# Performance work log

Measured on AMD Instinct MI355X. Metric: run time of the kernel, lower is better.

Reference implementation:

```python
import jax, jax.numpy as jnp
import numpy as np

NUM_HEADS = 28
HEAD_DIM = 128
NUM_KV_HEADS = 4
N_REP = NUM_HEADS // NUM_KV_HEADS  # 7
ROPE_THETA = 1000000.0
CUR_IND = 0  # prefill into empty cache
_K_MASK = float(jnp.finfo(jnp.bfloat16).min)


def _rope_sincos(position_ids, head_dim, theta):
    # position_ids: (B, T) int -> sin, cos: (B, T, head_dim//2)
    half = head_dim // 2
    fraction = jnp.arange(half, dtype=jnp.float32) / half
    timescale = theta ** fraction  # (half,)
    ang = position_ids[..., None].astype(jnp.float32) / timescale
    return jnp.sin(ang), jnp.cos(ang)


def _apply_rope(x, sin, cos):
    # x: (B, T, N, H); sin/cos: (B, T, H//2)
    half = x.shape[-1] // 2
    x1, x2 = x[..., :half], x[..., half:]
    s, c = sin[:, :, None, :], cos[:, :, None, :]
    return jnp.concatenate([x1 * c - x2 * s, x2 * c + x1 * s], axis=-1).astype(x.dtype)


def setup_inputs() -> dict:
    key = jax.random.key(0)
    ks = jax.random.split(key, 8)
    B, T, D = 2, 1024, 3584
    KVD = NUM_KV_HEADS * HEAD_DIM  # 512
    sd = 1.0 / np.sqrt(D)
    return {
        "x": jax.random.normal(ks[0], (B, T, D), jnp.float32),
        "segment_ids": jnp.ones((B, T), jnp.int32),
        "k_cache": jnp.zeros((B, T, NUM_KV_HEADS, HEAD_DIM), jnp.float32),
        "v_cache": jnp.zeros((B, T, NUM_KV_HEADS, HEAD_DIM), jnp.float32),
        "Wq": jax.random.normal(ks[1], (D, D), jnp.float32) * sd,
        "bq": jax.random.normal(ks[2], (D,), jnp.float32) * 0.01,
        "Wk": jax.random.normal(ks[3], (D, KVD), jnp.float32) * sd,
        "bk": jax.random.normal(ks[4], (KVD,), jnp.float32) * 0.01,
        "Wv": jax.random.normal(ks[5], (D, KVD), jnp.float32) * sd,
        "bv": jax.random.normal(ks[6], (KVD,), jnp.float32) * 0.01,
        "Wo": jax.random.normal(ks[7], (D, D), jnp.float32) * sd,
    }


def reference(x, segment_ids, k_cache, v_cache, Wq, bq, Wk, bk, Wv, bv, Wo):
    b, t, _ = x.shape
    cache_size = k_cache.shape[1]
    scale = HEAD_DIM ** -0.5

    q = (x @ Wq + bq).reshape(b, t, NUM_HEADS, HEAD_DIM)
    k = (x @ Wk + bk).reshape(b, t, NUM_KV_HEADS, HEAD_DIM)
    v = (x @ Wv + bv).reshape(b, t, NUM_KV_HEADS, HEAD_DIM)

    # left pads and positions (cache.start_ind initialized <0 -> becomes left_pads)
    valid = segment_ids != 0
    left_pads = jnp.sum(jnp.cumsum(valid, axis=-1) == 0, axis=-1).astype(jnp.int32)  # (B,)
    start_ind = left_pads
    position_ids = (jnp.cumsum(valid, axis=-1) - 1).astype(jnp.int32) + CUR_IND  # (B, T)

    sin, cos = _rope_sincos(position_ids, HEAD_DIM, ROPE_THETA)
    q = _apply_rope(q, sin, cos)
    k = _apply_rope(k, sin, cos)

    # write into KV cache at cur_ind (prefill: overwrites [0:t])
    k_cache = jax.lax.dynamic_update_slice(k_cache, k, (0, CUR_IND, 0, 0))
    v_cache = jax.lax.dynamic_update_slice(v_cache, v, (0, CUR_IND, 0, 0))

    q_gqa = q.reshape(b, t, NUM_KV_HEADS, N_REP, HEAD_DIM)
    attn_logits = jnp.einsum('BTKGH,BSKH->BTSKG', q_gqa, k_cache) * scale

    q_pos = CUR_IND + jnp.arange(t, dtype=jnp.int32)[None, :] - start_ind[:, None]  # (B,T)
    ts = jnp.arange(cache_size, dtype=jnp.int32)
    kv_segment_ids = (ts[None, :] >= start_ind[:, None]) & (ts[None, :] < CUR_IND + t)  # (B,S)
    k_pos = ts[None, :] - start_ind[:, None]  # (B,S)
    causal_mask = k_pos[:, None, :] <= q_pos[:, :, None]          # (B,T,S)
    segment_mask = kv_segment_ids[:, None, :] == segment_ids[:, :, None]  # (B,T,S)
    final_mask = (causal_mask & segment_mask)[:, :, :, None, None]  # (B,T,S,1,1)

    attn_logits = jnp.where(final_mask, attn_logits, _K_MASK)
    attn_weights = jax.nn.softmax(attn_logits.astype(jnp.float32), axis=2).astype(attn_logits.dtype)

    qkv = jnp.einsum('BTSKG,BSKH->BTKGH', attn_weights, v_cache)
    qkv = qkv.reshape(b, t, NUM_HEADS * HEAD_DIM)
    return qkv @ Wo
```

## Files before the change

kernel.cpp:

```cpp
#include <hip/hip_runtime.h>
#include <hip/hip_bf16.h>
#include <stdint.h>

#define T_SEQ 1024
#define DMODEL 3584
#define KVDIM 512
#define NQH 28
#define NKVH 4
#define NREP 7
#define HD 128
#define NTOT 4608
#define BATCH 2
#define MROWS 2048
#define KMASK (-3.3895314e38f)

typedef __attribute__((ext_vector_type(8))) short short8;
typedef __attribute__((ext_vector_type(4))) float f32x4;

#define SB()       asm volatile("s_barrier" ::: "memory")
#define WAIT_VM0() asm volatile("s_waitcnt vmcnt(0)" ::: "memory")

__device__ __forceinline__ short8 ld_s8(const __hip_bfloat16* p) {
    return *reinterpret_cast<const short8*>(p);
}

__device__ __forceinline__ f32x4 mfma16(short8 a, short8 b, f32x4 c) {
    return __builtin_amdgcn_mfma_f32_16x16x32_bf16(a, b, c, 0, 0, 0);
}

__device__ __forceinline__ void gload_lds16(const __hip_bfloat16* g, __hip_bfloat16* l) {
    __builtin_amdgcn_global_load_lds(
        (const __attribute__((address_space(1))) unsigned int*)g,
        (__attribute__((address_space(3))) unsigned int*)l,
        16, 0, 0);
}

__global__ void scan_kernel(const int* __restrict__ seg, int* __restrict__ pos_ids,
                            int* __restrict__ left_pads) {
    int b = blockIdx.x;
    int t = threadIdx.x;
    __shared__ int cum[T_SEQ];
    __shared__ int lp;
    if (t == 0) lp = 0;
    cum[t] = (seg[b * T_SEQ + t] != 0) ? 1 : 0;
    __syncthreads();
    for (int off = 1; off < T_SEQ; off <<= 1) {
        int add = (t >= off) ? cum[t - off] : 0;
        __syncthreads();
        cum[t] += add;
        __syncthreads();
    }
    pos_ids[b * T_SEQ + t] = cum[t] - 1;
    if (cum[t] == 0) atomicAdd(&lp, 1);
    __syncthreads();
    if (t == 0) left_pads[b] = lp;
}

__global__ void convert_bf16(const float* __restrict__ x, __hip_bfloat16* __restrict__ xb, int n) {
    int i = (blockIdx.x * blockDim.x + threadIdx.x) * 4;
    if (i >= n) return;
    float4 v = *reinterpret_cast<const float4*>(x + i);
    union { __hip_bfloat16 h[4]; uint2 u; } o;
    o.h[0] = __float2bfloat16(v.x);
    o.h[1] = __float2bfloat16(v.y);
    o.h[2] = __float2bfloat16(v.z);
    o.h[3] = __float2bfloat16(v.w);
    *reinterpret_cast<uint2*>(xb + i) = o.u;
}

__global__ void transpose_convert(const float* __restrict__ W, __hip_bfloat16* __restrict__ WT,
                                  int K, int N) {
    __shared__ float tile[32][33];
    int n0 = blockIdx.x * 32, k0 = blockIdx.y * 32;
    int tx = threadIdx.x, ty = threadIdx.y;
#pragma unroll
    for (int j = 0; j < 4; j++)
        tile[ty + j * 8][tx] = W[(size_t)(k0 + ty + j * 8) * N + n0 + tx];
    __syncthreads();
#pragma unroll
    for (int j = 0; j < 4; j++)
        WT[(size_t)(n0 + ty + j * 8) * K + k0 + tx] = __float2bfloat16(tile[tx][ty + j * 8]);
}

__global__ void transpose_v(const __hip_bfloat16* __restrict__ qkv, __hip_bfloat16* __restrict__ vbT) {
    __shared__ __hip_bfloat16 tile[32][33];
    int c0 = blockIdx.x * 32;
    int s0 = blockIdx.y * 32;
    int b = blockIdx.z;
    int tx = threadIdx.x, ty = threadIdx.y;
#pragma unroll
    for (int j = 0; j < 4; j++)
        tile[ty + j * 8][tx] = qkv[(size_t)(b * T_SEQ + s0 + ty + j * 8) * NTOT + DMODEL + KVDIM + c0 + tx];
    __syncthreads();
#pragma unroll
    for (int j = 0; j < 4; j++)
        vbT[((size_t)b * KVDIM + c0 + ty + j * 8) * T_SEQ + s0 + tx] = tile[tx][ty + j * 8];
}

__global__ void rope_kernel(__hip_bfloat16* __restrict__ qkv, const int* __restrict__ pos_ids) {
    int row = blockIdx.x;
    int tid = threadIdx.x;
    __shared__ float sc[2][64];
    float fpos = (float)pos_ids[row];
    if (tid < 64) {
        float freq = exp2f((float)tid * (-0.31143076632024816f));
        float ang = fpos * freq;
        sc[0][tid] = sinf(ang);
        sc[1][tid] = cosf(ang);
    }
    __syncthreads();
    __hip_bfloat16* rp = qkv + (size_t)row * NTOT;
    for (int p = tid; p < 32 * 64; p += 256) {
        int hh = p >> 6;
        int j = p & 63;
        int cb = (hh < NQH) ? hh * HD : DMODEL + (hh - NQH) * HD;
        float s = sc[0][j], c = sc[1][j];
        float x1 = __bfloat162float(rp[cb + j]);
        float x2 = __bfloat162float(rp[cb + j + 64]);
        rp[cb + j] = __float2bfloat16(x1 * c - x2 * s);
        rp[cb + j + 64] = __float2bfloat16(x2 * c + x1 * s);
    }
}

template <int MODE>
__global__ __launch_bounds__(512, 2) void gemm256(
    const __hip_bfloat16* __restrict__ A, const __hip_bfloat16* __restrict__ BT,
    int M, int N, int K, int nbx,
    const float* __restrict__ bq, const float* __restrict__ bk, const float* __restrict__ bv,
    __hip_bfloat16* __restrict__ Cb, float* __restrict__ Cf) {
    __shared__ __hip_bfloat16 As[2][256 * 64];
    __shared__ __hip_bfloat16 Bs[2][256 * 64];
    int tid = threadIdx.x;
    int wv = tid >> 6, lane = tid & 63;
    int wr = wv >> 2, wc = wv & 3;
    int r16 = lane & 15, g4 = lane >> 4;
    int nwg = gridDim.x;
    int sb = ((int)blockIdx.x & 7) * (nwg >> 3) + ((int)blockIdx.x >> 3);
    int bx = sb % nbx, by = sb / nbx;
    int bm = by * 256, bn = bx * 256;
    int nt = K >> 6;

    int lrow = lane >> 3;
    int srcoff = ((lane & 7) * 8) ^ (lrow * 8);

    auto stageA = [&](int buf, int t) {
        const __hip_bfloat16* src = A + (size_t)t * 64 + srcoff;
#pragma unroll
        for (int h = 0; h < 2; h++)
#pragma unroll
            for (int i = 0; i < 2; i++) {
                int r0 = h * 128 + wv * 16 + i * 8;
                gload_lds16(src + (size_t)(bm + r0 + lrow) * K, &As[buf][r0 * 64]);
            }
    };
    auto stageB = [&](int buf, int t) {
        const __hip_bfloat16* src = BT + (size_t)t * 64 + srcoff;
#pragma unroll
        for (int h = 0; h < 2; h++)
#pragma unroll
            for (int i = 0; i < 2; i++) {
                int r0 = h * 128 + wv * 16 + i * 8;
                gload_lds16(src + (size_t)(bn + r0 + lrow) * K, &Bs[buf][r0 * 64]);
            }
    };
    int swz = (r16 & 7) << 3;

    f32x4 acc[8][4] = {};
    stageA(0, 0);
    stageB(0, 0);

    for (int w = 0; w < nt; w++) {
        int buf = w & 1;
        WAIT_VM0();
        SB();
        short8 aF[4][2], bF0[2][2], bF1[2][2];
#pragma unroll
        for (int mi = 0; mi < 4; mi++)
#pragma unroll
            for (int ks = 0; ks < 2; ks++) {
                int row = wr * 128 + mi * 16 + r16;
                aF[mi][ks] = ld_s8(&As[buf][row * 64 + ((ks * 32 + g4 * 8) ^ swz)]);
            }
#pragma unroll
        for (int ni = 0; ni < 2; ni++)
#pragma unroll
            for (int ks = 0; ks < 2; ks++) {
                int row = wc * 64 + ni * 16 + r16;
                bF0[ni][ks] = ld_s8(&Bs[buf][row * 64 + ((ks * 32 + g4 * 8) ^ swz)]);
            }
        if (w + 1 < nt) stageA(buf ^ 1, w + 1);
        SB();
        __builtin_amdgcn_s_setprio(1);
#pragma unroll
        for (int mi = 0; mi < 4; mi++)
#pragma unroll
            for (int ni = 0; ni < 2; ni++) {
                acc[mi][ni] = mfma16(aF[mi][0], bF0[ni][0], acc[mi][ni]);
                acc[mi][ni] = mfma16(aF[mi][1], bF0[ni][1], acc[mi][ni]);
            }
        __builtin_amdgcn_s_setprio(0);
        SB();
#pragma unroll
        for (int ni = 0; ni < 2; ni++)
#pragma unroll
            for (int ks = 0; ks < 2; ks++) {
                int row = wc * 64 + (2 + ni) * 16 + r16;
                bF1[ni][ks] = ld_s8(&Bs[buf][row * 64 + ((ks * 32 + g4 * 8) ^ swz)]);
            }
        if (w + 1 < nt) stageB(buf ^ 1, w + 1);
        SB();
        __builtin_amdgcn_s_setprio(1);
#pragma unroll
        for (int mi = 0; mi < 4; mi++)
#pragma unroll
            for (int ni = 0; ni < 2; ni++) {
                acc[mi][2 + ni] = mfma16(aF[mi][0], bF1[ni][0], acc[mi][2 + ni]);
                acc[mi][2 + ni] = mfma16(aF[mi][1], bF1[ni][1], acc[mi][2 + ni]);
            }
        __builtin_amdgcn_s_setprio(0);
        SB();
#pragma unroll
        for (int mi = 0; mi < 4; mi++)
#pragma unroll
            for (int ks = 0; ks < 2; ks++) {
                int row = wr * 128 + 64 + mi * 16 + r16;
                aF[mi][ks] = ld_s8(&As[buf][row * 64 + ((ks * 32 + g4 * 8) ^ swz)]);
            }
        SB();
        __builtin_amdgcn_s_setprio(1);
#pragma unroll
        for (int mi = 0; mi < 4; mi++)
#pragma unroll
            for (int ni = 0; ni < 2; ni++) {
                acc[4 + mi][ni] = mfma16(aF[mi][0], bF0[ni][0], acc[4 + mi][ni]);
                acc[4 + mi][ni] = mfma16(aF[mi][1], bF0[ni][1], acc[4 + mi][ni]);
            }
        __builtin_amdgcn_s_setprio(0);
        SB();
        __builtin_amdgcn_s_setprio(1);
#pragma unroll
        for (int mi = 0; mi < 4; mi++)
#pragma unroll
            for (int ni = 0; ni < 2; ni++) {
                acc[4 + mi][2 + ni] = mfma16(aF[mi][0], bF1[ni][0], acc[4 + mi][2 + ni]);
                acc[4 + mi][2 + ni] = mfma16(aF[mi][1], bF1[ni][1], acc[4 + mi][2 + ni]);
            }
        __builtin_amdgcn_s_setprio(0);
    }
#pragma unroll
    for (int m = 0; m < 8; m++) {
#pragma unroll
        for (int n = 0; n < 4; n++) {
            int row0 = bm + wr * 128 + m * 16 + g4 * 4;
            int col = bn + wc * 64 + n * 16 + r16;
            float badd = 0.0f;
            if (MODE == 0)
                badd = (col < DMODEL) ? bq[col]
                       : (col < DMODEL + KVDIM ? bk[col - DMODEL] : bv[col - DMODEL - KVDIM]);
#pragma unroll
            for (int reg = 0; reg < 4; reg++) {
                float v = acc[m][n][reg] + badd;
                if (MODE == 0)
                    Cb[(size_t)(row0 + reg) * N + col] = __float2bfloat16(v);
                else
                    Cf[(size_t)(row0 + reg) * N + col] = v;
            }
        }
    }
}

__global__ __launch_bounds__(448, 4) void attn_kernel(
    const __hip_bfloat16* __restrict__ qkv, const __hip_bfloat16* __restrict__ vbT,
    const int* __restrict__ seg, const int* __restrict__ left_pads,
    __hip_bfloat16* __restrict__ attn_out) {
    int qt_raw = blockIdx.x;
    int kvh = blockIdx.y;
    int b = blockIdx.z;
    int qt = (b == 1) ? 63 - qt_raw : qt_raw;
    int tid = threadIdx.x;
    int w = tid >> 6;
    int lane = tid & 63;
    int r = lane & 15, g = lane >> 4;
    int h = kvh * NREP + w;
    int start = left_pads[b];
    const float scale = 0.08838834764831845f;

    __shared__ __hip_bfloat16 Kt[2][64 * 128];
    __shared__ __hip_bfloat16 Vt[2][128 * 64];
    __shared__ __hip_bfloat16 Ps[NREP][16 * 64];

    const __hip_bfloat16* Qp = qkv + (size_t)(b * T_SEQ + qt * 16 + r) * NTOT + h * HD;
    short8 qf[4];
#pragma unroll
    for (int kc = 0; kc < 4; kc++) qf[kc] = ld_s8(Qp + kc * 32 + g * 8);

    int qrow = qt * 16 + r;
    int segq = seg[b * T_SEQ + qrow];
    int qpos = qrow - start;

    float m_run = -__builtin_inff();
    float l_part = 0.0f;
    f32x4 acc[8] = {};

    const __hip_bfloat16* Kg = qkv + (size_t)(b * T_SEQ) * NTOT + DMODEL + kvh * HD;
    const __hip_bfloat16* Vg = vbT + ((size_t)b * KVDIM + kvh * HD) * T_SEQ;
    int nt = qt / 4 + 1;

    auto stage = [&](int buf, int t) {
        int s0 = t * 64;
        for (int i = w; i < 16; i += NREP) {
            int slot = i * 64 + lane;
            int row = slot >> 4;
            int c = ((slot & 15) << 4) ^ ((row & 7) << 4);
            gload_lds16(Kg + (size_t)(s0 + row) * NTOT + (c >> 1), &Kt[buf][i * 512]);
        }
        for (int i = w; i < 16; i += NREP) {
            int slot = i * 64 + lane;
            int d = slot >> 3;
            int c = ((slot & 7) << 4) ^ ((d & 7) << 4);
            gload_lds16(Vg + (size_t)d * T_SEQ + s0 + (c >> 1), &Vt[buf][i * 512]);
        }
    };

    stage(0, 0);
    __syncthreads();
    int buf = 0;
    for (int t = 0; t < nt; t++) {
        if (t + 1 < nt) stage(buf ^ 1, t + 1);
        int s0 = t * 64;
        f32x4 sacc[4] = {};
#pragma unroll
        for (int n = 0; n < 4; n++) {
#pragma unroll
            for (int kc = 0; kc < 4; kc++) {
                int col = (kc * 32 + g * 8) ^ ((r & 7) << 3);
                short8 kf = ld_s8(&Kt[buf][(n * 16 + r) * 128 + col]);
                sacc[n] = mfma16(kf, qf[kc], sacc[n]);
            }
        }
        float p[16];
        float mt = -__builtin_inff();
#pragma unroll
        for (int n = 0; n < 4; n++)
#pragma unroll
            for (int reg = 0; reg < 4; reg++) {
                int kv = s0 + n * 16 + g * 4 + reg;
                float val = sacc[n][reg] * scale;
                bool ok = (kv - start <= qpos) && (((kv >= start) ? 1 : 0) == segq);
                val = ok ? val : KMASK;
                p[n * 4 + reg] = val;
                mt = fmaxf(mt, val);
            }
        mt = fmaxf(mt, __shfl_xor(mt, 16, 64));
        mt = fmaxf(mt, __shfl_xor(mt, 32, 64));
        if (!__all(mt <= m_run + 8.0f)) {
            float mn = fmaxf(m_run, mt);
            float fac = __expf(m_run - mn);
            m_run = mn;
            l_part *= fac;
            float facr[4];
#pragma unroll
            for (int reg = 0; reg < 4; reg++) facr[reg] = __shfl(fac, g * 4 + reg, 64);
#pragma unroll
            for (int h7 = 0; h7 < 8; h7++)
#pragma unroll
                for (int reg = 0; reg < 4; reg++)
                    acc[h7][reg] *= facr[reg];
        }
#pragma unroll
        for (int i = 0; i < 16; i++) {
            p[i] = __expf(p[i] - m_run);
            l_part += p[i];
        }
#pragma unroll
        for (int n = 0; n < 4; n++) {
            union { __hip_bfloat16 h[4]; uint2 u; } pk;
#pragma unroll
            for (int reg = 0; reg < 4; reg++) pk.h[reg] = __float2bfloat16(p[n * 4 + reg]);
            int col = (n * 16 + g * 4) ^ ((r & 7) << 3);
            *reinterpret_cast<uint2*>(&Ps[w][r * 64 + col]) = pk.u;
        }
#pragma unroll
        for (int kc = 0; kc < 2; kc++) {
            int colp = (kc * 32 + g * 8) ^ ((r & 7) << 3);
            short8 a_pv = ld_s8(&Ps[w][r * 64 + colp]);
#pragma unroll
            for (int h7 = 0; h7 < 8; h7++) {
                int d = h7 * 16 + r;
                int colv = (kc * 32 + g * 8) ^ ((r & 7) << 3);
                short8 vf = ld_s8(&Vt[buf][d * 64 + colv]);
                acc[h7] = mfma16(a_pv, vf, acc[h7]);
            }
        }
        __syncthreads();
        buf ^= 1;
    }
    l_part += __shfl_xor(l_part, 16, 64);
    l_part += __shfl_xor(l_part, 32, 64);
    float invl[4];
#pragma unroll
    for (int reg = 0; reg < 4; reg++) invl[reg] = 1.0f / __shfl(l_part, g * 4 + reg, 64);
#pragma unroll
    for (int h7 = 0; h7 < 8; h7++)
#pragma unroll
        for (int reg = 0; reg < 4; reg++)
            attn_out[(size_t)(b * T_SEQ + qt * 16 + g * 4 + reg) * DMODEL + h * HD + h7 * 16 + r] =
                __float2bfloat16(acc[h7][reg] * invl[reg]);
}

extern "C" void kernel_launch(void* const* d_in, const int* in_sizes, int n_in,
                              void* d_out, int out_size, void* d_ws, size_t ws_size,
                              hipStream_t stream) {
    const float* x = (const float*)d_in[0];
    const int* seg = (const int*)d_in[1];
    const float* Wq = (const float*)d_in[4];
    const float* bq = (const float*)d_in[5];
    const float* Wk = (const float*)d_in[6];
    const float* bk = (const float*)d_in[7];
    const float* Wv = (const float*)d_in[8];
    const float* bv = (const float*)d_in[9];
    const float* Wo = (const float*)d_in[10];
    float* out = (float*)d_out;

    uint8_t* ws = (uint8_t*)d_ws;
    size_t off = 0;
    auto alloc = [&](size_t bytes) -> void* {
        void* p = ws + off;
        off += (bytes + 255) & ~(size_t)255;
        return p;
    };
    int* pos_ids = (int*)alloc(MROWS * sizeof(int));
    int* left_pads = (int*)alloc(16 * sizeof(int));
    __hip_bfloat16* xb = (__hip_bfloat16*)alloc((size_t)MROWS * DMODEL * 2);
    __hip_bfloat16* WqkvT = (__hip_bfloat16*)alloc((size_t)NTOT * DMODEL * 2);
    __hip_bfloat16* WoT = (__hip_bfloat16*)alloc((size_t)DMODEL * DMODEL * 2);
    __hip_bfloat16* qkv = (__hip_bfloat16*)alloc((size_t)MROWS * NTOT * 2);
    __hip_bfloat16* vbT = (__hip_bfloat16*)alloc((size_t)BATCH * KVDIM * T_SEQ * 2);
    __hip_bfloat16* attn = (__hip_bfloat16*)alloc((size_t)MROWS * DMODEL * 2);

    scan_kernel<<<BATCH, T_SEQ, 0, stream>>>(seg, pos_ids, left_pads);
    convert_bf16<<<(MROWS * DMODEL / 4 + 255) / 256, 256, 0, stream>>>(x, xb, MROWS * DMODEL);
    transpose_convert<<<dim3(DMODEL / 32, DMODEL / 32), dim3(32, 8), 0, stream>>>(Wq, WqkvT, DMODEL, DMODEL);
    transpose_convert<<<dim3(KVDIM / 32, DMODEL / 32), dim3(32, 8), 0, stream>>>(
        Wk, WqkvT + (size_t)DMODEL * DMODEL, DMODEL, KVDIM);
    transpose_convert<<<dim3(KVDIM / 32, DMODEL / 32), dim3(32, 8), 0, stream>>>(
        Wv, WqkvT + (size_t)(DMODEL + KVDIM) * DMODEL, DMODEL, KVDIM);
    transpose_convert<<<dim3(DMODEL / 32, DMODEL / 32), dim3(32, 8), 0, stream>>>(Wo, WoT, DMODEL, DMODEL);
    gemm256<0><<<dim3((NTOT / 256) * (MROWS / 256)), 512, 0, stream>>>(
        xb, WqkvT, MROWS, NTOT, DMODEL, NTOT / 256, bq, bk, bv, qkv, nullptr);
    rope_kernel<<<MROWS, 256, 0, stream>>>(qkv, pos_ids);
    transpose_v<<<dim3(KVDIM / 32, T_SEQ / 32, BATCH), dim3(32, 8), 0, stream>>>(qkv, vbT);
    attn_kernel<<<dim3(T_SEQ / 16, NKVH, BATCH), 448, 0, stream>>>(qkv, vbT, seg, left_pads, attn);
    gemm256<1><<<dim3((DMODEL / 256) * (MROWS / 256)), 512, 0, stream>>>(
        attn, WoT, MROWS, DMODEL, DMODEL, DMODEL / 256, nullptr, nullptr, nullptr, nullptr, out);
}
```

Baseline: 469.7 us.

## Retile GEMMs to 128xBN tiles sized so grids exactly fill 256 CUs

Replaces the fixed 256x256, 8-wave GEMM with a templated 128xBN kernel: BN=288 with 9 waves for the QKV projection and BN=224 with 7 waves for the output projection. Each launch is exactly 256 workgroups, matching the MI355X CU count, which removes the partial-wave tail of the old 144- and 112-block grids. Each wave now covers a 128x32 output slice instead of 128x64, so there are fewer MFMAs per LDS fragment load and less data reuse. Launch bounds drop to one block per SM.

```diff
diff --git a/kernel.cpp b/kernel.cpp
--- a/kernel.cpp
+++ b/kernel.cpp
@@ -122,22 +122,24 @@
     }
 }
 
-template <int MODE>
-__global__ __launch_bounds__(512, 2) void gemm256(
+template <int BN, int NW, int MODE>
+__global__ __launch_bounds__(NW * 64, 1) void gemmX(
     const __hip_bfloat16* __restrict__ A, const __hip_bfloat16* __restrict__ BT,
     int M, int N, int K, int nbx,
     const float* __restrict__ bq, const float* __restrict__ bk, const float* __restrict__ bv,
     __hip_bfloat16* __restrict__ Cb, float* __restrict__ Cf) {
-    __shared__ __hip_bfloat16 As[2][256 * 64];
-    __shared__ __hip_bfloat16 Bs[2][256 * 64];
+    constexpr int BM = 128;
+    constexpr int NCHA = BM / 8;
+    constexpr int NCHB = BN / 8;
+    __shared__ __hip_bfloat16 As[2][BM * 64];
+    __shared__ __hip_bfloat16 Bs[2][BN * 64];
     int tid = threadIdx.x;
     int wv = tid >> 6, lane = tid & 63;
-    int wr = wv >> 2, wc = wv & 3;
     int r16 = lane & 15, g4 = lane >> 4;
     int nwg = gridDim.x;
     int sb = ((int)blockIdx.x & 7) * (nwg >> 3) + ((int)blockIdx.x >> 3);
     int bx = sb % nbx, by = sb / nbx;
-    int bm = by * 256, bn = bx * 256;
+    int bm = by * BM, bn = bx * BN;
     int nt = K >> 6;
 
     int lrow = lane >> 3;
@@ -146,26 +148,24 @@
     auto stageA = [&](int buf, int t) {
         const __hip_bfloat16* src = A + (size_t)t * 64 + srcoff;
 #pragma unroll
-        for (int h = 0; h < 2; h++)
-#pragma unroll
-            for (int i = 0; i < 2; i++) {
-                int r0 = h * 128 + wv * 16 + i * 8;
-                gload_lds16(src + (size_t)(bm + r0 + lrow) * K, &As[buf][r0 * 64]);
-            }
+        for (int c = 0; c < NCHA; c += NW) {
+            int cc = c + wv;
+            if (cc < NCHA)
+                gload_lds16(src + (size_t)(bm + cc * 8 + lrow) * K, &As[buf][cc * 512]);
+        }
     };
     auto stageB = [&](int buf, int t) {
         const __hip_bfloat16* src = BT + (size_t)t * 64 + srcoff;
 #pragma unroll
-        for (int h = 0; h < 2; h++)
-#pragma unroll
-            for (int i = 0; i < 2; i++) {
-                int r0 = h * 128 + wv * 16 + i * 8;
-                gload_lds16(src + (size_t)(bn + r0 + lrow) * K, &Bs[buf][r0 * 64]);
-            }
+        for (int c = 0; c < NCHB; c += NW) {
+            int cc = c + wv;
+            if (cc < NCHB)
+                gload_lds16(src + (size_t)(bn + cc * 8 + lrow) * K, &Bs[buf][cc * 512]);
+        }
     };
     int swz = (r16 & 7) << 3;
 
-    f32x4 acc[8][4] = {};
+    f32x4 acc[8][2] = {};
     stageA(0, 0);
     stageB(0, 0);
 
@@ -173,21 +173,17 @@
         int buf = w & 1;
         WAIT_VM0();
         SB();
-        short8 aF[4][2], bF0[2][2], bF1[2][2];
+        short8 aLo[4][2], aHi[4][2], bF[2][2];
 #pragma unroll
         for (int mi = 0; mi < 4; mi++)
 #pragma unroll
-            for (int ks = 0; ks < 2; ks++) {
-                int row = wr * 128 + mi * 16 + r16;
-                aF[mi][ks] = ld_s8(&As[buf][row * 64 + ((ks * 32 + g4 * 8) ^ swz)]);
-            }
+            for (int ks = 0; ks < 2; ks++)
+                aLo[mi][ks] = ld_s8(&As[buf][(mi * 16 + r16) * 64 + ((ks * 32 + g4 * 8) ^ swz)]);
 #pragma unroll
         for (int ni = 0; ni < 2; ni++)
 #pragma unroll
-            for (int ks = 0; ks < 2; ks++) {
-                int row = wc * 64 + ni * 16 + r16;
-                bF0[ni][ks] = ld_s8(&Bs[buf][row * 64 + ((ks * 32 + g4 * 8) ^ swz)]);
-            }
+            for (int ks = 0; ks < 2; ks++)
+                bF[ni][ks] = ld_s8(&Bs[buf][(wv * 32 + ni * 16 + r16) * 64 + ((ks * 32 + g4 * 8) ^ swz)]);
         if (w + 1 < nt) stageA(buf ^ 1, w + 1);
         SB();
         __builtin_amdgcn_s_setprio(1);
@@ -195,18 +191,16 @@
         for (int mi = 0; mi < 4; mi++)
 #pragma unroll
             for (int ni = 0; ni < 2; ni++) {
-                acc[mi][ni] = mfma16(aF[mi][0], bF0[ni][0], acc[mi][ni]);
-                acc[mi][ni] = mfma16(aF[mi][1], bF0[ni][1], acc[mi][ni]);
+                acc[mi][ni] = mfma16(aLo[mi][0], bF[ni][0], acc[mi][ni]);
+                acc[mi][ni] = mfma16(aLo[mi][1], bF[ni][1], acc[mi][ni]);
             }
         __builtin_amdgcn_s_setprio(0);
         SB();
 #pragma unroll
-        for (int ni = 0; ni < 2; ni++)
-#pragma unroll
-            for (int ks = 0; ks < 2; ks++) {
-                int row = wc * 64 + (2 + ni) * 16 + r16;
-                bF1[ni][ks] = ld_s8(&Bs[buf][row * 64 + ((ks * 32 + g4 * 8) ^ swz)]);
-            }
+        for (int mi = 0; mi < 4; mi++)
+#pragma unroll
+            for (int ks = 0; ks < 2; ks++)
+                aHi[mi][ks] = ld_s8(&As[buf][((64 + mi * 16 + r16)) * 64 + ((ks * 32 + g4 * 8) ^ swz)]);
         if (w + 1 < nt) stageB(buf ^ 1, w + 1);
         SB();
         __builtin_amdgcn_s_setprio(1);
@@ -214,45 +208,17 @@
         for (int mi = 0; mi < 4; mi++)
 #pragma unroll
             for (int ni = 0; ni < 2; ni++) {
-                acc[mi][2 + ni] = mfma16(aF[mi][0], bF1[ni][0], acc[mi][2 + ni]);
-                acc[mi][2 + ni] = mfma16(aF[mi][1], bF1[ni][1], acc[mi][2 + ni]);
+                acc[4 + mi][ni] = mfma16(aHi[mi][0], bF[ni][0], acc[4 + mi][ni]);
+                acc[4 + mi][ni] = mfma16(aHi[mi][1], bF[ni][1], acc[4 + mi][ni]);
             }
         __builtin_amdgcn_s_setprio(0);
-        SB();
-#pragma unroll
-        for (int mi = 0; mi < 4; mi++)
-#pragma unroll
-            for (int ks = 0; ks < 2; ks++) {
-                int row = wr * 128 + 64 + mi * 16 + r16;
-                aF[mi][ks] = ld_s8(&As[buf][row * 64 + ((ks * 32 + g4 * 8) ^ swz)]);
-            }
-        SB();
-        __builtin_amdgcn_s_setprio(1);
-#pragma unroll
-        for (int mi = 0; mi < 4; mi++)
-#pragma unroll
-            for (int ni = 0; ni < 2; ni++) {
-                acc[4 + mi][ni] = mfma16(aF[mi][0], bF0[ni][0], acc[4 + mi][ni]);
-                acc[4 + mi][ni] = mfma16(aF[mi][1], bF0[ni][1], acc[4 + mi][ni]);
-            }
-        __builtin_amdgcn_s_setprio(0);
-        SB();
-        __builtin_amdgcn_s_setprio(1);
-#pragma unroll
-        for (int mi = 0; mi < 4; mi++)
-#pragma unroll
-            for (int ni = 0; ni < 2; ni++) {
-                acc[4 + mi][2 + ni] = mfma16(aF[mi][0], bF1[ni][0], acc[4 + mi][2 + ni]);
-                acc[4 + mi][2 + ni] = mfma16(aF[mi][1], bF1[ni][1], acc[4 + mi][2 + ni]);
-            }
-        __builtin_amdgcn_s_setprio(0);
     }
 #pragma unroll
     for (int m = 0; m < 8; m++) {
 #pragma unroll
-        for (int n = 0; n < 4; n++) {
-            int row0 = bm + wr * 128 + m * 16 + g4 * 4;
-            int col = bn + wc * 64 + n * 16 + r16;
+        for (int n = 0; n < 2; n++) {
+            int row0 = bm + m * 16 + g4 * 4;
+            int col = bn + wv * 32 + n * 16 + r16;
             float badd = 0.0f;
             if (MODE == 0)
                 badd = (col < DMODEL) ? bq[col]
@@ -446,11 +412,11 @@
     transpose_convert<<<dim3(KVDIM / 32, DMODEL / 32), dim3(32, 8), 0, stream>>>(
         Wv, WqkvT + (size_t)(DMODEL + KVDIM) * DMODEL, DMODEL, KVDIM);
     transpose_convert<<<dim3(DMODEL / 32, DMODEL / 32), dim3(32, 8), 0, stream>>>(Wo, WoT, DMODEL, DMODEL);
-    gemm256<0><<<dim3((NTOT / 256) * (MROWS / 256)), 512, 0, stream>>>(
-        xb, WqkvT, MROWS, NTOT, DMODEL, NTOT / 256, bq, bk, bv, qkv, nullptr);
+    gemmX<288, 9, 0><<<dim3(256), 9 * 64, 0, stream>>>(
+        xb, WqkvT, MROWS, NTOT, DMODEL, NTOT / 288, bq, bk, bv, qkv, nullptr);
     rope_kernel<<<MROWS, 256, 0, stream>>>(qkv, pos_ids);
     transpose_v<<<dim3(KVDIM / 32, T_SEQ / 32, BATCH), dim3(32, 8), 0, stream>>>(qkv, vbT);
     attn_kernel<<<dim3(T_SEQ / 16, NKVH, BATCH), 448, 0, stream>>>(qkv, vbT, seg, left_pads, attn);
-    gemm256<1><<<dim3((DMODEL / 256) * (MROWS / 256)), 512, 0, stream>>>(
-        attn, WoT, MROWS, DMODEL, DMODEL, DMODEL / 256, nullptr, nullptr, nullptr, nullptr, out);
-}
+    gemmX<224, 7, 1><<<dim3(256), 7 * 64, 0, stream>>>(
+        attn, WoT, MROWS, DMODEL, DMODEL, DMODEL / 224, nullptr, nullptr, nullptr, nullptr, out);
+}
```

Result: faster. 407.2 us (-13.3%).
